# Kernel optimization log

Measured on AMD Instinct MI355X. Metric: run time of the kernel, lower is better.

Reference implementation:

```python
import jax, jax.numpy as jnp
import numpy as np
import math

MAX_LEN = 5000

def _build_pe(d_feat: int, dtype=jnp.float32) -> jnp.ndarray:
    # d_model rounded up to even, as in run_once
    d_model = int(math.ceil(d_feat / 2) * 2)
    pos = jnp.arange(MAX_LEN, dtype=dtype)[:, None]                       # [L,1]
    div = jnp.exp(jnp.arange(0, d_model, 2, dtype=dtype)
                  * (-math.log(10000.0) / d_model))                       # [d_model/2]
    pe = jnp.zeros((MAX_LEN, d_model), dtype=dtype)
    pe = pe.at[:, 0::2].set(jnp.sin(pos * div))
    pe = pe.at[:, 1::2].set(jnp.cos(pos * div))
    return pe

def setup_inputs() -> dict:
    key = jax.random.key(0)
    k1, k2 = jax.random.split(key)
    B, S, D = 32, 4096, 256
    nodes = jax.random.normal(k1, (B, S, D), dtype=jnp.float32)
    num_nodes = jax.random.randint(k2, (B,), 0, S, dtype=jnp.int64 if jax.config.read('jax_enable_x64') else jnp.int32)
    return {"nodes": nodes, "num_nodes": num_nodes}

def reference(nodes, num_nodes):
    # torch: pe.roll(center,0)[i] = pe[(i-center) % MAX_LEN]; add to nodes[b,:center+1]
    B, S, D = nodes.shape
    pe = _build_pe(D, nodes.dtype)                                        # [L, d_model]
    i = jnp.arange(S)                                                     # [S]
    idx = (i[None, :] - num_nodes[:, None]) % MAX_LEN                     # [B,S]
    mask = i[None, :] <= num_nodes[:, None]                               # [B,S]
    add = pe[idx, :D]                                                     # [B,S,D] gather
    return nodes + jnp.where(mask[:, :, None], add, jnp.zeros((), nodes.dtype))
```

## Files before the change

### kernel.cpp

```cpp
#include <hip/hip_runtime.h>
#include <math.h>


typedef float v4f __attribute__((ext_vector_type(4)));

__global__ __launch_bounds__(256) void rpe_kernel(const float* __restrict__ nodes,
                                                  const int* __restrict__ num_nodes,
                                                  float* __restrict__ out,
                                                  const int total4) {
    const int tid = blockIdx.x * blockDim.x + threadIdx.x;
    if (tid >= total4) return;

    const int d4 = tid & 63;
    const int s  = (tid >> 6) & 4095;
    const int b  = tid >> 18;

    const int nn = num_nodes[b];

    v4f v = reinterpret_cast<const v4f*>(nodes)[tid];

    if (s <= nn) {
        int r = s - nn;
        int p = (r < 0) ? r + 5000 : r;
        const float pf = (float)p;

        const float cexp   = -0.051905126482062035f;
        const float inv2pi = 0.15915494309189535f;
        const float f0 = exp2f(cexp * (float)(4 * d4)) * inv2pi;
        const float f1 = exp2f(cexp * (float)(4 * d4 + 2)) * inv2pi;

        float r0 = pf * f0;  r0 -= floorf(r0);
        float r1 = pf * f1;  r1 -= floorf(r1);

        v.x += __builtin_amdgcn_sinf(r0);
        v.y += __builtin_amdgcn_cosf(r0);
        v.z += __builtin_amdgcn_sinf(r1);
        v.w += __builtin_amdgcn_cosf(r1);
    }

    reinterpret_cast<v4f*>(out)[tid] = v;
}

extern "C" void kernel_launch(void* const* d_in, const int* in_sizes, int n_in,
                              void* d_out, int out_size, void* d_ws, size_t ws_size,
                              hipStream_t stream) {
    const float* nodes     = (const float*)d_in[0];
    const int*   num_nodes = (const int*)d_in[1];
    float*       out       = (float*)d_out;

    const int total4 = out_size / 4;
    const int block  = 256;
    const int grid   = (total4 + block - 1) / block;

    rpe_kernel<<<grid, block, 0, stream>>>(nodes, num_nodes, out, total4);
}
```

Before: 223.4 us.

## Unroll four vectors per thread with nontemporal loads/stores and branchless PE add

```diff
diff --git a/kernel.cpp b/kernel.cpp
--- a/kernel.cpp
+++ b/kernel.cpp
@@ -4,41 +4,76 @@
 
 typedef float v4f __attribute__((ext_vector_type(4)));
 
-__global__ __launch_bounds__(256) void rpe_kernel(const float* __restrict__ nodes,
-                                                  const int* __restrict__ num_nodes,
-                                                  float* __restrict__ out,
-                                                  const int total4) {
-    const int tid = blockIdx.x * blockDim.x + threadIdx.x;
-    if (tid >= total4) return;
+#define BLOCK 256
+#define UNROLL 4
 
-    const int d4 = tid & 63;
-    const int s  = (tid >> 6) & 4095;
-    const int b  = tid >> 18;
+__device__ __forceinline__ v4f pe_add(v4f v, int idx, int nn, float f0, float f1) {
+    const int s = (idx >> 6) & 4095;
+    int r = s - nn;
+    int p = (r < 0) ? r + 5000 : r;
+    const float pf = (float)p;
+    float r0 = pf * f0;  r0 -= floorf(r0);
+    float r1 = pf * f1;  r1 -= floorf(r1);
+    const float m = (s <= nn) ? 1.0f : 0.0f;
+    v.x = fmaf(m, __builtin_amdgcn_sinf(r0), v.x);
+    v.y = fmaf(m, __builtin_amdgcn_cosf(r0), v.y);
+    v.z = fmaf(m, __builtin_amdgcn_sinf(r1), v.z);
+    v.w = fmaf(m, __builtin_amdgcn_cosf(r1), v.w);
+    return v;
+}
 
-    const int nn = num_nodes[b];
+template <bool EXACT>
+__global__ __launch_bounds__(BLOCK) void rpe_kernel(const float* __restrict__ nodes,
+                                                    const int* __restrict__ num_nodes,
+                                                    float* __restrict__ out,
+                                                    const int total4) {
+    const int base = blockIdx.x * (BLOCK * UNROLL) + threadIdx.x;
 
-    v4f v = reinterpret_cast<const v4f*>(nodes)[tid];
+    const int d4 = base & 63;
+    const float cexp   = -0.051905126482062035f;
+    const float inv2pi = 0.15915494309189535f;
+    const float f0 = exp2f(cexp * (float)(4 * d4)) * inv2pi;
+    const float f1 = exp2f(cexp * (float)(4 * d4 + 2)) * inv2pi;
 
-    if (s <= nn) {
-        int r = s - nn;
-        int p = (r < 0) ? r + 5000 : r;
-        const float pf = (float)p;
+    const v4f* __restrict__ in4  = reinterpret_cast<const v4f*>(nodes);
+    v4f* __restrict__       out4 = reinterpret_cast<v4f*>(out);
 
-        const float cexp   = -0.051905126482062035f;
-        const float inv2pi = 0.15915494309189535f;
-        const float f0 = exp2f(cexp * (float)(4 * d4)) * inv2pi;
-        const float f1 = exp2f(cexp * (float)(4 * d4 + 2)) * inv2pi;
+    if (EXACT) {
+        const int i0 = base;
+        const int i1 = base + BLOCK;
+        const int i2 = base + 2 * BLOCK;
+        const int i3 = base + 3 * BLOCK;
 
-        float r0 = pf * f0;  r0 -= floorf(r0);
-        float r1 = pf * f1;  r1 -= floorf(r1);
+        v4f v0 = __builtin_nontemporal_load(in4 + i0);
+        v4f v1 = __builtin_nontemporal_load(in4 + i1);
+        v4f v2 = __builtin_nontemporal_load(in4 + i2);
+        v4f v3 = __builtin_nontemporal_load(in4 + i3);
+        const int n0 = num_nodes[__builtin_amdgcn_readfirstlane(i0 >> 18)];
+        const int n1 = num_nodes[__builtin_amdgcn_readfirstlane(i1 >> 18)];
+        const int n2 = num_nodes[__builtin_amdgcn_readfirstlane(i2 >> 18)];
+        const int n3 = num_nodes[__builtin_amdgcn_readfirstlane(i3 >> 18)];
 
-        v.x += __builtin_amdgcn_sinf(r0);
-        v.y += __builtin_amdgcn_cosf(r0);
-        v.z += __builtin_amdgcn_sinf(r1);
-        v.w += __builtin_amdgcn_cosf(r1);
+        v0 = pe_add(v0, i0, n0, f0, f1);
+        v1 = pe_add(v1, i1, n1, f0, f1);
+        v2 = pe_add(v2, i2, n2, f0, f1);
+        v3 = pe_add(v3, i3, n3, f0, f1);
+
+        __builtin_nontemporal_store(v0, out4 + i0);
+        __builtin_nontemporal_store(v1, out4 + i1);
+        __builtin_nontemporal_store(v2, out4 + i2);
+        __builtin_nontemporal_store(v3, out4 + i3);
+    } else {
+        #pragma unroll
+        for (int j = 0; j < UNROLL; ++j) {
+            const int idx = base + j * BLOCK;
+            if (idx < total4) {
+                v4f v = __builtin_nontemporal_load(in4 + idx);
+                const int nn = num_nodes[__builtin_amdgcn_readfirstlane(idx >> 18)];
+                v = pe_add(v, idx, nn, f0, f1);
+                __builtin_nontemporal_store(v, out4 + idx);
+            }
+        }
     }
-
-    reinterpret_cast<v4f*>(out)[tid] = v;
 }
 
 extern "C" void kernel_launch(void* const* d_in, const int* in_sizes, int n_in,
@@ -49,8 +84,11 @@
     float*       out       = (float*)d_out;
 
     const int total4 = out_size / 4;
-    const int block  = 256;
-    const int grid   = (total4 + block - 1) / block;
+    const int grid   = (total4 + BLOCK * UNROLL - 1) / (BLOCK * UNROLL);
 
-    rpe_kernel<<<grid, block, 0, stream>>>(nodes, num_nodes, out, total4);
+    if (total4 % (BLOCK * UNROLL) == 0) {
+        rpe_kernel<true><<<grid, BLOCK, 0, stream>>>(nodes, num_nodes, out, total4);
+    } else {
+        rpe_kernel<false><<<grid, BLOCK, 0, stream>>>(nodes, num_nodes, out, total4);
+    }
 }
```

Result: no change. 220.6 us (-1.3%).
